# Optimization experiments

Measured on AMD Instinct MI355X. Metric: run time of the kernel, lower is better.

The kernel has to match this reference:

```python
import jax, jax.numpy as jnp
import numpy as np

TOPK = 8


def setup_inputs() -> dict:
    key = jax.random.key(0)
    k1, k2, k3 = jax.random.split(key, 3)
    B, LT, LV, D = 8, 4096, 4096, 1024
    return {
        "text_feats": jax.random.normal(k1, (B, LT, D), dtype=jnp.float32),
        "visual_feats": jax.random.normal(k2, (B, LV, D), dtype=jnp.float32),
        "W_key": jax.random.normal(k3, (D, D), dtype=jnp.float32) / np.sqrt(D).astype(np.float32),
        "b_key": jnp.zeros((D,), dtype=jnp.float32),
    }


def reference(text_feats, visual_feats, W_key, b_key):
    topk = TOPK
    B, LT, D = text_feats.shape
    # Text key nodes: L2 norm scores -> top-k -> gather. [B, topk, D]
    scores = jnp.linalg.norm(text_feats, axis=-1)            # [B, LT]
    _, idx = jax.lax.top_k(scores, topk)                      # [B, topk]
    text_keys = jnp.take_along_axis(text_feats, idx[:, :, None], axis=1)
    # Visual scores are mean(ones)=const in inference => torch.topk picks first topk indices.
    visual_keys = visual_feats[:, :topk, :]                   # [B, topk, D]
    # Tiny cross attention over key nodes.
    tq = text_keys @ W_key.T + b_key                          # nn.Linear: x @ W^T + b
    sim = jnp.einsum('btk,bvk->btv', tq, visual_keys)         # [B, topk, topk]
    hyper_edges = jax.nn.softmax(sim, axis=-1)
    text_out = jnp.einsum('btv,bvd->btd', hyper_edges, visual_keys)
    visual_out = jnp.einsum('btv,btd->bvd', hyper_edges, text_keys)
    # Pad both outputs back to text sequence length.
    pad = LT - topk
    text_out = jnp.pad(text_out, ((0, 0), (0, pad), (0, 0)))
    visual_out = jnp.pad(visual_out, ((0, 0), (0, pad), (0, 0)))
    return text_out, visual_out
```

## Files before the change

kernel.cpp:

```cpp
#include <hip/hip_runtime.h>

#define BATCH 8
#define LT 4096
#define LV 4096
#define DIM 1024
#define TOPK 8

__global__ __launch_bounds__(256) void k_norm_zero(const float* __restrict__ tf,
                                                   float* __restrict__ norms,
                                                   float* __restrict__ out) {
    int blk = blockIdx.x;
    if (blk < 8192) {
        int wave = threadIdx.x >> 6;
        int lane = threadIdx.x & 63;
        int row  = blk * 4 + wave;
        const float4* p = (const float4*)(tf + (size_t)row * DIM);
        float acc = 0.f;
#pragma unroll
        for (int j = 0; j < 4; ++j) {
            float4 v = p[lane + 64 * j];
            acc += v.x * v.x + v.y * v.y + v.z * v.z + v.w * v.w;
        }
#pragma unroll
        for (int o = 32; o > 0; o >>= 1) acc += __shfl_down(acc, o, 64);
        if (lane == 0) norms[row] = acc;
    } else {
        int zb  = blk - 8192;
        int seg = zb & 15;
        int sub = zb >> 4;
        float4* base = (float4*)out + (size_t)seg * 1048576 + 2048;
        const int len = 1046528;
        float4 z = make_float4(0.f, 0.f, 0.f, 0.f);
        for (int i = sub * 256 + (int)threadIdx.x; i < len; i += 128 * 256)
            base[i] = z;
    }
}

__global__ __launch_bounds__(256) void k_topk(const float* __restrict__ norms,
                                              int* __restrict__ idx_out) {
    __shared__ float s[LT];
    __shared__ float rv[256];
    __shared__ int   ri[256];
    int b = blockIdx.x, tid = threadIdx.x;
    for (int i = tid; i < LT; i += 256) s[i] = norms[b * LT + i];
    __syncthreads();
    for (int r = 0; r < TOPK; ++r) {
        float bv = -2.f; int bi = 0x7fffffff;
        for (int i = tid; i < LT; i += 256) {
            float v = s[i];
            if (v > bv) { bv = v; bi = i; }
        }
        rv[tid] = bv; ri[tid] = bi;
        __syncthreads();
        for (int o = 128; o > 0; o >>= 1) {
            if (tid < o) {
                float v2 = rv[tid + o]; int i2 = ri[tid + o];
                if (v2 > rv[tid] || (v2 == rv[tid] && i2 < ri[tid])) {
                    rv[tid] = v2; ri[tid] = i2;
                }
            }
            __syncthreads();
        }
        if (tid == 0) { idx_out[b * TOPK + r] = ri[0]; s[ri[0]] = -1.f; }
        __syncthreads();
    }
}

__global__ __launch_bounds__(256) void k_tq(const float* __restrict__ tf,
                                            const float* __restrict__ W,
                                            const float* __restrict__ bias,
                                            const int* __restrict__ idx,
                                            float* __restrict__ tq) {
    int b = blockIdx.y;
    int chunk = blockIdx.x;
    __shared__ float tk[TOPK][DIM];
    for (int t = 0; t < TOPK; ++t) {
        const float4* src = (const float4*)(tf + ((size_t)b * LT + idx[b * TOPK + t]) * DIM);
        float4* dst = (float4*)tk[t];
        for (int i = threadIdx.x; i < DIM / 4; i += 256) dst[i] = src[i];
    }
    __syncthreads();
    int dloc = threadIdx.x & 63;
    int tp   = threadIdx.x >> 6;
    int d = chunk * 64 + dloc;
    const float4* wrow = (const float4*)(W + (size_t)d * DIM);
    const float4* tk0  = (const float4*)tk[tp];
    const float4* tk1  = (const float4*)tk[tp + 4];
    float acc0 = 0.f, acc1 = 0.f;
    for (int k = 0; k < DIM / 4; ++k) {
        float4 w = wrow[k];
        float4 a = tk0[k], c = tk1[k];
        acc0 += w.x * a.x + w.y * a.y + w.z * a.z + w.w * a.w;
        acc1 += w.x * c.x + w.y * c.y + w.z * c.z + w.w * c.w;
    }
    float bb = bias[d];
    tq[(b * TOPK + tp) * DIM + d]     = acc0 + bb;
    tq[(b * TOPK + tp + 4) * DIM + d] = acc1 + bb;
}

__global__ __launch_bounds__(256) void k_attn(const float* __restrict__ tf,
                                              const float* __restrict__ vf,
                                              const float* __restrict__ tq,
                                              const int* __restrict__ idx,
                                              float* __restrict__ out) {
    int b = blockIdx.x, tid = threadIdx.x;
    __shared__ float vk[TOPK][DIM];
    __shared__ float sim[TOPK][TOPK];
    __shared__ float he[TOPK][TOPK];
    {
        const float4* src = (const float4*)(vf + (size_t)b * LV * DIM);
        float4* dst = (float4*)vk;
        for (int i = tid; i < TOPK * DIM / 4; i += 256) dst[i] = src[i];
    }
    __syncthreads();
    int wave = tid >> 6, lane = tid & 63;
    for (int p = wave * 16; p < wave * 16 + 16; ++p) {
        int t = p >> 3, v = p & 7;
        const float4* q  = (const float4*)(tq + (b * TOPK + t) * DIM);
        const float4* vv = (const float4*)vk[v];
        float acc = 0.f;
#pragma unroll
        for (int j = 0; j < 4; ++j) {
            float4 a = q[lane + 64 * j];
            float4 c = vv[lane + 64 * j];
            acc += a.x * c.x + a.y * c.y + a.z * c.z + a.w * c.w;
        }
#pragma unroll
        for (int o = 32; o > 0; o >>= 1) acc += __shfl_down(acc, o, 64);
        if (lane == 0) sim[t][v] = acc;
    }
    __syncthreads();
    if (tid < TOPK) {
        float m = -1e30f;
#pragma unroll
        for (int v = 0; v < TOPK; ++v) m = fmaxf(m, sim[tid][v]);
        float e[TOPK], ssum = 0.f;
#pragma unroll
        for (int v = 0; v < TOPK; ++v) { e[v] = expf(sim[tid][v] - m); ssum += e[v]; }
        float inv = 1.f / ssum;
#pragma unroll
        for (int v = 0; v < TOPK; ++v) he[tid][v] = e[v] * inv;
    }
    __syncthreads();
    float* to = out + (size_t)b * LT * DIM;
    float* vo = out + (size_t)(BATCH + b) * LT * DIM;
    for (int i = tid; i < TOPK * DIM; i += 256) {
        int t = i >> 10, d = i & 1023;
        float acc = 0.f;
#pragma unroll
        for (int v = 0; v < TOPK; ++v) acc += he[t][v] * vk[v][d];
        to[t * DIM + d] = acc;
    }
    const float* tfb = tf + (size_t)b * LT * DIM;
    int rows[TOPK];
#pragma unroll
    for (int t = 0; t < TOPK; ++t) rows[t] = idx[b * TOPK + t];
    for (int i = tid; i < TOPK * DIM; i += 256) {
        int v = i >> 10, d = i & 1023;
        float acc = 0.f;
#pragma unroll
        for (int t = 0; t < TOPK; ++t) acc += he[t][v] * tfb[(size_t)rows[t] * DIM + d];
        vo[v * DIM + d] = acc;
    }
}

extern "C" void kernel_launch(void* const* d_in, const int* in_sizes, int n_in,
                              void* d_out, int out_size, void* d_ws, size_t ws_size,
                              hipStream_t stream) {
    const float* tf   = (const float*)d_in[0];
    const float* vf   = (const float*)d_in[1];
    const float* W    = (const float*)d_in[2];
    const float* bias = (const float*)d_in[3];
    float* out = (float*)d_out;
    float* ws  = (float*)d_ws;
    float* norms = ws;
    int*   idx   = (int*)(ws + 32768);
    float* tq    = ws + 32768 + 64;

    k_norm_zero<<<10240, 256, 0, stream>>>(tf, norms, out);
    k_topk<<<8, 256, 0, stream>>>(norms, idx);
    k_tq<<<dim3(16, 8), 256, 0, stream>>>(tf, W, bias, idx, tq);
    k_attn<<<8, 256, 0, stream>>>(tf, vf, tq, idx, out);
}
```

Baseline: 502.5 us.

## Fuse top-k into consumer kernels and interleave norm and zero-fill blocks

Drops the separate top-k launch. Each k_tq and k_attn block now recomputes the per-batch top-k selection from the norms, which adds redundant work to every block but saves one launch and its dependency gap. The norm/zero kernel now interleaves norm blocks with zero-fill blocks so memory reads and writes are mixed across the grid. k_attn also stages the gathered text rows in shared memory, and the k_tq inner loop gets an unroll pragma.

```diff
diff --git a/kernel.cpp b/kernel.cpp
--- a/kernel.cpp
+++ b/kernel.cpp
@@ -6,42 +6,9 @@
 #define DIM 1024
 #define TOPK 8
 
-__global__ __launch_bounds__(256) void k_norm_zero(const float* __restrict__ tf,
-                                                   float* __restrict__ norms,
-                                                   float* __restrict__ out) {
-    int blk = blockIdx.x;
-    if (blk < 8192) {
-        int wave = threadIdx.x >> 6;
-        int lane = threadIdx.x & 63;
-        int row  = blk * 4 + wave;
-        const float4* p = (const float4*)(tf + (size_t)row * DIM);
-        float acc = 0.f;
-#pragma unroll
-        for (int j = 0; j < 4; ++j) {
-            float4 v = p[lane + 64 * j];
-            acc += v.x * v.x + v.y * v.y + v.z * v.z + v.w * v.w;
-        }
-#pragma unroll
-        for (int o = 32; o > 0; o >>= 1) acc += __shfl_down(acc, o, 64);
-        if (lane == 0) norms[row] = acc;
-    } else {
-        int zb  = blk - 8192;
-        int seg = zb & 15;
-        int sub = zb >> 4;
-        float4* base = (float4*)out + (size_t)seg * 1048576 + 2048;
-        const int len = 1046528;
-        float4 z = make_float4(0.f, 0.f, 0.f, 0.f);
-        for (int i = sub * 256 + (int)threadIdx.x; i < len; i += 128 * 256)
-            base[i] = z;
-    }
-}
-
-__global__ __launch_bounds__(256) void k_topk(const float* __restrict__ norms,
-                                              int* __restrict__ idx_out) {
-    __shared__ float s[LT];
-    __shared__ float rv[256];
-    __shared__ int   ri[256];
-    int b = blockIdx.x, tid = threadIdx.x;
+__device__ __forceinline__ void block_topk(const float* __restrict__ norms, int b,
+                                           float* s, float* rv, int* ri, int* tidx) {
+    int tid = threadIdx.x;
     for (int i = tid; i < LT; i += 256) s[i] = norms[b * LT + i];
     __syncthreads();
     for (int r = 0; r < TOPK; ++r) {
@@ -61,32 +28,69 @@
             }
             __syncthreads();
         }
-        if (tid == 0) { idx_out[b * TOPK + r] = ri[0]; s[ri[0]] = -1.f; }
+        if (tid == 0) { tidx[r] = ri[0]; s[ri[0]] = -1.f; }
         __syncthreads();
     }
 }
 
+__global__ __launch_bounds__(256) void k_norm_zero(const float* __restrict__ tf,
+                                                   float* __restrict__ norms,
+                                                   float* __restrict__ out) {
+    int blk = blockIdx.x;
+    int g = blk / 5, r = blk % 5;
+    if (r < 4) {
+        int n = g * 4 + r;
+        int wave = threadIdx.x >> 6;
+        int lane = threadIdx.x & 63;
+        int row  = n * 4 + wave;
+        const float4* p = (const float4*)(tf + (size_t)row * DIM);
+        float acc = 0.f;
+#pragma unroll
+        for (int j = 0; j < 4; ++j) {
+            float4 v = p[lane + 64 * j];
+            acc += v.x * v.x + v.y * v.y + v.z * v.z + v.w * v.w;
+        }
+#pragma unroll
+        for (int o = 32; o > 0; o >>= 1) acc += __shfl_down(acc, o, 64);
+        if (lane == 0) norms[row] = acc;
+    } else {
+        int f   = g;
+        int seg = f & 15;
+        int sub = f >> 4;
+        float4* base = (float4*)out + (size_t)seg * 1048576 + 2048;
+        const int len = 1046528;
+        float4 z = make_float4(0.f, 0.f, 0.f, 0.f);
+        for (int i = sub * 256 + (int)threadIdx.x; i < len; i += 128 * 256)
+            base[i] = z;
+    }
+}
+
 __global__ __launch_bounds__(256) void k_tq(const float* __restrict__ tf,
+                                            const float* __restrict__ norms,
                                             const float* __restrict__ W,
                                             const float* __restrict__ bias,
-                                            const int* __restrict__ idx,
                                             float* __restrict__ tq) {
-    int b = blockIdx.y;
-    int chunk = blockIdx.x;
+    __shared__ float s[LT];
+    __shared__ float rv[256];
+    __shared__ int   ri[256];
+    __shared__ int   tidx[TOPK];
     __shared__ float tk[TOPK][DIM];
+    int b = blockIdx.y, chunk = blockIdx.x, tid = threadIdx.x;
+    block_topk(norms, b, s, rv, ri, tidx);
     for (int t = 0; t < TOPK; ++t) {
-        const float4* src = (const float4*)(tf + ((size_t)b * LT + idx[b * TOPK + t]) * DIM);
+        const float4* src = (const float4*)(tf + ((size_t)b * LT + tidx[t]) * DIM);
         float4* dst = (float4*)tk[t];
-        for (int i = threadIdx.x; i < DIM / 4; i += 256) dst[i] = src[i];
+        for (int i = tid; i < DIM / 4; i += 256) dst[i] = src[i];
     }
     __syncthreads();
-    int dloc = threadIdx.x & 63;
-    int tp   = threadIdx.x >> 6;
+    int dloc = tid & 63;
+    int tp   = tid >> 6;
     int d = chunk * 64 + dloc;
     const float4* wrow = (const float4*)(W + (size_t)d * DIM);
     const float4* tk0  = (const float4*)tk[tp];
     const float4* tk1  = (const float4*)tk[tp + 4];
     float acc0 = 0.f, acc1 = 0.f;
+#pragma unroll 4
     for (int k = 0; k < DIM / 4; ++k) {
         float4 w = wrow[k];
         float4 a = tk0[k], c = tk1[k];
@@ -100,17 +104,28 @@
 
 __global__ __launch_bounds__(256) void k_attn(const float* __restrict__ tf,
                                               const float* __restrict__ vf,
+                                              const float* __restrict__ norms,
                                               const float* __restrict__ tq,
-                                              const int* __restrict__ idx,
                                               float* __restrict__ out) {
-    int b = blockIdx.x, tid = threadIdx.x;
+    __shared__ float s[LT];
+    __shared__ float rv[256];
+    __shared__ int   ri[256];
+    __shared__ int   tidx[TOPK];
     __shared__ float vk[TOPK][DIM];
+    __shared__ float tk[TOPK][DIM];
     __shared__ float sim[TOPK][TOPK];
     __shared__ float he[TOPK][TOPK];
+    int b = blockIdx.x, tid = threadIdx.x;
+    block_topk(norms, b, s, rv, ri, tidx);
     {
         const float4* src = (const float4*)(vf + (size_t)b * LV * DIM);
         float4* dst = (float4*)vk;
         for (int i = tid; i < TOPK * DIM / 4; i += 256) dst[i] = src[i];
+        for (int t = 0; t < TOPK; ++t) {
+            const float4* ts = (const float4*)(tf + ((size_t)b * LT + tidx[t]) * DIM);
+            float4* td = (float4*)tk[t];
+            for (int i = tid; i < DIM / 4; i += 256) td[i] = ts[i];
+        }
     }
     __syncthreads();
     int wave = tid >> 6, lane = tid & 63;
@@ -151,15 +166,11 @@
         for (int v = 0; v < TOPK; ++v) acc += he[t][v] * vk[v][d];
         to[t * DIM + d] = acc;
     }
-    const float* tfb = tf + (size_t)b * LT * DIM;
-    int rows[TOPK];
-#pragma unroll
-    for (int t = 0; t < TOPK; ++t) rows[t] = idx[b * TOPK + t];
     for (int i = tid; i < TOPK * DIM; i += 256) {
         int v = i >> 10, d = i & 1023;
         float acc = 0.f;
 #pragma unroll
-        for (int t = 0; t < TOPK; ++t) acc += he[t][v] * tfb[(size_t)rows[t] * DIM + d];
+        for (int t = 0; t < TOPK; ++t) acc += he[t][v] * tk[t][d];
         vo[v * DIM + d] = acc;
     }
 }
@@ -174,11 +185,9 @@
     float* out = (float*)d_out;
     float* ws  = (float*)d_ws;
     float* norms = ws;
-    int*   idx   = (int*)(ws + 32768);
     float* tq    = ws + 32768 + 64;
 
     k_norm_zero<<<10240, 256, 0, stream>>>(tf, norms, out);
-    k_topk<<<8, 256, 0, stream>>>(norms, idx);
-    k_tq<<<dim3(16, 8), 256, 0, stream>>>(tf, W, bias, idx, tq);
-    k_attn<<<8, 256, 0, stream>>>(tf, vf, tq, idx, out);
+    k_tq<<<dim3(16, 8), 256, 0, stream>>>(tf, norms, W, bias, tq);
+    k_attn<<<8, 256, 0, stream>>>(tf, vf, norms, tq, out);
 }
```

Measured after the change: 503.1 us. Within noise of the previous version (+0.1%).
